# Optimization experiments

Measured on AMD Instinct MI355X. Metric: run time of the kernel, lower is better.

## Reference

```python
import jax, jax.numpy as jnp
import numpy as np

EMBED_DIM = 1024
NUM_HEADS = 16
HEAD_DIM = EMBED_DIM // NUM_HEADS
SEG_LENS = [1024, 2048, 4096]
DIL_RATIOS = [1, 2, 4]
NEG = -1e8  # lse fill value used by sparse_to_dense


def setup_inputs() -> dict:
    root = jax.random.key(0)
    ks = jax.random.split(root, 12)
    B, L, E = 1, 4096, EMBED_DIM
    s = 0.02
    return {
        "query": jax.random.normal(ks[0], (B, L, E), jnp.float32),
        "key": jax.random.normal(ks[1], (B, L, E), jnp.float32),
        "value": jax.random.normal(ks[2], (B, L, E), jnp.float32),
        "Wq": jax.random.normal(ks[3], (E, E), jnp.float32) * s,
        "bq": jnp.zeros((E,), jnp.float32),
        "Wk": jax.random.normal(ks[4], (E, E), jnp.float32) * s,
        "bk": jnp.zeros((E,), jnp.float32),
        "Wv": jax.random.normal(ks[5], (E, E), jnp.float32) * s,
        "bv": jnp.zeros((E,), jnp.float32),
        "Wo": jax.random.normal(ks[6], (E, E), jnp.float32) * s,
        "bo": jnp.zeros((E,), jnp.float32),
    }


def _branch(q, k, v, sl, dr, L):
    """One (segment_length, dilated_ratio) branch.
    q,k,v: (B, L, H, D). Returns dense out (B, H, L, D) and lse (B, H, L).
    """
    B = q.shape[0]
    H, D = NUM_HEADS, HEAD_DIM
    sl = min(sl, L)
    pad = (-L) % sl
    if pad:
        pw = ((0, 0), (0, pad), (0, 0), (0, 0))
        q, k, v = jnp.pad(q, pw), jnp.pad(k, pw), jnp.pad(v, pw)
    n = (L + pad) // sl  # segments
    qs = q.reshape(B * n, sl, H, D)
    ks = k.reshape(B * n, sl, H, D)
    vs = v.reshape(B * n, sl, H, D)
    # dense_to_sparse: head j (group r = j // (H//dr)) keeps positions i*dr + r
    hg = H // dr
    g = sl // dr
    grp = jnp.arange(H) // hg                      # (H,)
    pos = jnp.arange(g)[:, None] * dr + grp[None]  # (g, H) dense positions
    hidx = jnp.arange(H)[None, :]
    sp = lambda x: x[:, pos, hidx, :]              # (B*n, g, H, D)
    qd, kd, vd = sp(qs), sp(ks), sp(vs)
    # causal attention within each sparse segment (flash_attn semantics)
    scores = jnp.einsum('bqhd,bkhd->bhqk', qd, kd) * (D ** -0.5)
    mask = jnp.tril(jnp.ones((g, g), bool))
    scores = jnp.where(mask, scores, -jnp.inf)
    lse = jax.nn.logsumexp(scores, axis=-1)        # (B*n, H, g)
    o = jnp.einsum('bhqk,bkhd->bqhd', jnp.exp(scores - lse[..., None]), vd)
    # sparse_to_dense: scatter back onto dense positions, NEG elsewhere
    hcol = jnp.arange(H)[:, None]                  # (H,1)
    od = jnp.zeros((B * n, H, sl, D), o.dtype).at[:, hcol, pos.T].set(
        o.transpose(0, 2, 1, 3))
    ld = jnp.zeros((B * n, H, sl), lse.dtype).at[:, hcol, pos.T].set(lse)
    ld = jnp.where(ld == 0.0, NEG, ld)  # matches masked_fill_(lse == 0, -1e8)
    od = od.reshape(B, n, H, sl, D).transpose(0, 2, 1, 3, 4)
    od = od.reshape(B, H, n * sl, D)[:, :, :L]
    ld = ld.reshape(B, n, H, sl).transpose(0, 2, 1, 3).reshape(B, H, n * sl)[:, :, :L]
    return od, ld


def reference(query, key, value, Wq, bq, Wk, bk, Wv, bv, Wo, bo):
    B, L, E = query.shape
    H, D = NUM_HEADS, HEAD_DIM
    q = (query @ Wq.T + bq).reshape(B, L, H, D)
    k = (key @ Wk.T + bk).reshape(B, L, H, D)
    v = (value @ Wv.T + bv).reshape(B, L, H, D)
    outs, lses = [], []
    for sl, dr in zip(SEG_LENS, DIL_RATIOS):
        o, l = _branch(q, k, v, sl, dr, L)
        outs.append(o)
        lses.append(l)
    lse_all = jnp.stack(lses, 0)[..., None]        # (nb, B, H, L, 1)
    m = lse_all.max(0)
    w = jnp.exp(lse_all - m)
    w = w / w.sum(0)                               # softmax merge weights
    w = jax.lax.stop_gradient(w)                   # torch computes under no_grad
    out = sum(o * wi.astype(o.dtype) for o, wi in zip(outs, w))  # (B,H,L,D)
    out = out.transpose(0, 2, 1, 3).reshape(B, L, E)
    return out @ Wo.T + bo
```

## Files before the change

kernel.cpp:

```cpp
#include <hip/hip_runtime.h>
#include <math.h>


#define L_SEQ 4096
#define EDIM  1024
#define NH    16
#define HD    64
#define GLEN  1024

typedef __bf16 bf16;
typedef __bf16 bf16x8 __attribute__((ext_vector_type(8)));
typedef __bf16 bf16x4 __attribute__((ext_vector_type(4)));
typedef short  s16x4  __attribute__((ext_vector_type(4)));
typedef float  f32x4  __attribute__((ext_vector_type(4)));

__device__ __forceinline__ void gload16(const bf16* g, bf16* l) {
  __builtin_amdgcn_global_load_lds(
      (__attribute__((address_space(1))) void*)(const_cast<bf16*>(g)),
      (__attribute__((address_space(3))) void*)(l),
      16, 0, 0);
}

__device__ __forceinline__ f32x4 mfma16x16x16_bf16(bf16x4 a, bf16x4 b, f32x4 c) {
#if defined(__HIP_DEVICE_COMPILE__)
  union { bf16x4 h; s16x4 s; } ua, ub;
  ua.h = a; ub.h = b;
  return __builtin_amdgcn_mfma_f32_16x16x16bf16_1k(ua.s, ub.s, c, 0, 0, 0);
#else
  (void)a; (void)b;
  return c;
#endif
}

__global__ __launch_bounds__(256) void cvt_kernel(
    const float* q, const float* k, const float* v,
    const float* wq, const float* wk, const float* wv, const float* wo,
    bf16* oq, bf16* ok, bf16* ov,
    bf16* owq, bf16* owk, bf16* owv, bf16* owo)
{
  const float* src; bf16* dst; int n;
  switch (blockIdx.y) {
    case 0: src = q;  dst = oq;  n = L_SEQ*EDIM; break;
    case 1: src = k;  dst = ok;  n = L_SEQ*EDIM; break;
    case 2: src = v;  dst = ov;  n = L_SEQ*EDIM; break;
    case 3: src = wq; dst = owq; n = EDIM*EDIM; break;
    case 4: src = wk; dst = owk; n = EDIM*EDIM; break;
    case 5: src = wv; dst = owv; n = EDIM*EDIM; break;
    default: src = wo; dst = owo; n = EDIM*EDIM; break;
  }
  int i = (blockIdx.x * 256 + threadIdx.x) * 8;
  if (i >= n) return;
  const float4* s4 = (const float4*)(src + i);
  float4 a = s4[0], b = s4[1];
  bf16x8 o = { (bf16)a.x, (bf16)a.y, (bf16)a.z, (bf16)a.w,
               (bf16)b.x, (bf16)b.y, (bf16)b.z, (bf16)b.w };
  *(bf16x8*)(dst + i) = o;
}

template <typename OutT>
__device__ __forceinline__ void gemm_body(const bf16* __restrict__ A,
                                          const bf16* __restrict__ W,
                                          const float* __restrict__ bias,
                                          OutT* __restrict__ C)
{
  constexpr int K = 1024;
  __shared__ __align__(16) bf16 lA[128 * 32];
  __shared__ __align__(16) bf16 lB[128 * 32];

  const int tid  = threadIdx.x;
  const int lane = tid & 63;
  const int w    = tid >> 6;
  const int quad = lane >> 4;
  const int l16  = lane & 15;
  const int wr   = w >> 1, wc = w & 1;
  const int row0 = blockIdx.y * 128;
  const int col0 = blockIdx.x * 128;

  f32x4 acc[4][4] = {};

  const int c0 = tid, c1 = tid + 256;
  const bf16* Ab0 = A + (size_t)(row0 + (c0 >> 2)) * K + (c0 & 3) * 8;
  const bf16* Ab1 = A + (size_t)(row0 + (c1 >> 2)) * K + (c1 & 3) * 8;
  const bf16* Bb0 = W + (size_t)(col0 + (c0 >> 2)) * K + (c0 & 3) * 8;
  const bf16* Bb1 = W + (size_t)(col0 + (c1 >> 2)) * K + (c1 & 3) * 8;
  bf16* lA0 = &lA[c0 * 8]; bf16* lA1 = &lA[c1 * 8];
  bf16* lB0 = &lB[c0 * 8]; bf16* lB1 = &lB[c1 * 8];

  for (int kt = 0; kt < K; kt += 32) {
    __syncthreads();
    gload16(Ab0 + kt, lA0);
    gload16(Ab1 + kt, lA1);
    gload16(Bb0 + kt, lB0);
    gload16(Bb1 + kt, lB1);
    __syncthreads();

    bf16x8 af[4], bfrag[4];
#pragma unroll
    for (int mi = 0; mi < 4; mi++)
      af[mi] = *(const bf16x8*)&lA[(wr * 64 + mi * 16 + l16) * 32 + quad * 8];
#pragma unroll
    for (int ni = 0; ni < 4; ni++)
      bfrag[ni] = *(const bf16x8*)&lB[(wc * 64 + ni * 16 + l16) * 32 + quad * 8];
#pragma unroll
    for (int mi = 0; mi < 4; mi++)
#pragma unroll
      for (int ni = 0; ni < 4; ni++)
        acc[mi][ni] = __builtin_amdgcn_mfma_f32_16x16x32_bf16(
            af[mi], bfrag[ni], acc[mi][ni], 0, 0, 0);
  }

#pragma unroll
  for (int mi = 0; mi < 4; mi++) {
#pragma unroll
    for (int ni = 0; ni < 4; ni++) {
      const int gcol = col0 + wc * 64 + ni * 16 + l16;
      const float bv = bias[gcol];
#pragma unroll
      for (int r = 0; r < 4; r++) {
        const int grow = row0 + wr * 64 + mi * 16 + quad * 4 + r;
        C[(size_t)grow * 1024 + gcol] = (OutT)(acc[mi][ni][r] + bv);
      }
    }
  }
}

__global__ __launch_bounds__(256) void gemm_qkv_kernel(
    const bf16* xq, const bf16* xk, const bf16* xv,
    const bf16* wq, const bf16* wk, const bf16* wv,
    const float* bq, const float* bk, const float* bv,
    bf16* q, bf16* k, bf16* v)
{
  const bf16 *A, *W; const float* bias; bf16* C;
  if (blockIdx.z == 0)      { A = xq; W = wq; bias = bq; C = q; }
  else if (blockIdx.z == 1) { A = xk; W = wk; bias = bk; C = k; }
  else                      { A = xv; W = wv; bias = bv; C = v; }
  gemm_body<bf16>(A, W, bias, C);
}

__global__ __launch_bounds__(256) void gemm_out_kernel(
    const bf16* A, const bf16* W, const float* bias, float* C)
{
  gemm_body<float>(A, W, bias, C);
}

__global__ __launch_bounds__(256) void reshape_kernel(
    const bf16* __restrict__ k, const bf16* __restrict__ v,
    bf16* kt0, bf16* kt1, bf16* kt2,
    bf16* vt0, bf16* vt1, bf16* vt2)
{
  __shared__ __align__(16) bf16 ltile[64 * 72];
  const int bid = blockIdx.x;
  int sl, dr, rem, shift; bf16 *ktb, *vtb;
  if (bid < 1024)      { sl = 1024; dr = 1; rem = bid;        ktb = kt0; vtb = vt0; shift = 4; }
  else if (bid < 1536) { sl = 2048; dr = 2; rem = bid - 1024; ktb = kt1; vtb = vt1; shift = 3; }
  else                 { sl = 4096; dr = 4; rem = bid - 1536; ktb = kt2; vtb = vt2; shift = 2; }
  const int ktile = rem & 15;
  const int h     = (rem >> 4) & 15;
  const int seg   = rem >> 8;
  const int grp   = h >> shift;
  const int segbase = seg * sl;
  const int tid = threadIdx.x;
  const size_t tOff = ((size_t)((seg * NH + h) * 16 + ktile)) * 4096;

  {
#pragma unroll
    for (int half = 0; half < 2; half++) {
      const int p   = tid + half * 256;
      const int kjl = p >> 3, dc = p & 7;
      const bf16* src = k + (size_t)(segbase + (ktile * 64 + kjl) * dr + grp) * EDIM + h * 64 + dc * 8;
      *(uint4*)(ktb + tOff + p * 8) = *(const uint4*)src;
    }
  }
  {
    const int i = tid >> 2, dc = tid & 3;
    const size_t p = (size_t)(segbase + (ktile * 64 + i) * dr + grp);
    const bf16* src = v + p * EDIM + h * 64 + dc * 16;
    *(uint4*)&ltile[i * 72 + dc * 16]     = *(const uint4*)(src);
    *(uint4*)&ltile[i * 72 + dc * 16 + 8] = *(const uint4*)(src + 8);
  }
  __syncthreads();
  {
    const int d = tid >> 2, kc = tid & 3;
    __align__(16) bf16 tmp[16];
#pragma unroll
    for (int j = 0; j < 16; j++) tmp[j] = ltile[(kc * 16 + j) * 72 + d];
    bf16* dst = vtb + tOff + d * 64 + kc * 16;
    *(uint4*)dst       = *(uint4*)&tmp[0];
    *(uint4*)(dst + 8) = *(uint4*)&tmp[8];
  }
}

__global__ __launch_bounds__(256) void attn_kernel(
    const bf16* __restrict__ qg,
    const bf16* kt0, const bf16* kt1, const bf16* kt2,
    const bf16* vt0, const bf16* vt1, const bf16* vt2,
    bf16* o0, bf16* o1, bf16* o2,
    float* l0, float* l1, float* l2)
{
  __shared__ __align__(16) bf16 lK[64 * 64];
  __shared__ __align__(16) bf16 lV[64 * 64];

  const int bid = blockIdx.x;
  int sl, dr, rem, shift;
  const bf16 *ktb, *vtb; bf16* ob; float* lseb;
  if (bid < 1024)      { sl = 1024; dr = 1; rem = bid;        ktb = kt0; vtb = vt0; ob = o0; lseb = l0; shift = 4; }
  else if (bid < 1536) { sl = 2048; dr = 2; rem = bid - 1024; ktb = kt1; vtb = vt1; ob = o1; lseb = l1; shift = 3; }
  else                 { sl = 4096; dr = 4; rem = bid - 1536; ktb = kt2; vtb = vt2; ob = o2; lseb = l2; shift = 2; }
  const int qt  = 15 - (rem & 15);
  const int h   = (rem >> 4) & 15;
  const int seg = rem >> 8;
  const int grp = h >> shift;
  const int segbase = seg * sl;

  const int tid = threadIdx.x, lane = tid & 63, w = tid >> 6;
  const int quad = lane >> 4, l16 = lane & 15;
  const int qs0 = qt * 64;
  const int qi_lane = qs0 + w * 16 + l16;

  bf16x8 qa0, qa1;
  {
    const size_t p = (size_t)(segbase + qi_lane * dr + grp);
    const bf16* qp = qg + p * EDIM + h * 64 + quad * 8;
    qa0 = *(const bf16x8*)(qp);
    qa1 = *(const bf16x8*)(qp + 32);
  }

  f32x4 Oa[4] = {};
  float m_r = -__builtin_inff(), l_r = 0.f;

  const bf16* kbase = ktb + ((size_t)((seg * NH + h) * 16)) * 4096;
  const bf16* vbase = vtb + ((size_t)((seg * NH + h) * 16)) * 4096;

  const int p0 = tid, p1 = tid + 256;
  const int s0 = (p0 >> 3) * 64 + (((p0 & 7) ^ ((p0 >> 3) & 7)) * 8);
  const int s1 = (p1 >> 3) * 64 + (((p1 & 7) ^ ((p1 >> 3) & 7)) * 8);

  uint4 rk0 = *(const uint4*)(kbase + p0 * 8);
  uint4 rk1 = *(const uint4*)(kbase + p1 * 8);
  uint4 rv0 = *(const uint4*)(vbase + p0 * 8);
  uint4 rv1 = *(const uint4*)(vbase + p1 * 8);

  for (int kt = 0; kt <= qt; kt++) {
    __syncthreads();
    *(uint4*)&lK[s0] = rk0;
    *(uint4*)&lK[s1] = rk1;
    *(uint4*)&lV[s0] = rv0;
    *(uint4*)&lV[s1] = rv1;
    if (kt < qt) {
      const bf16* kT = kbase + (size_t)(kt + 1) * 4096;
      const bf16* vT = vbase + (size_t)(kt + 1) * 4096;
      rk0 = *(const uint4*)(kT + p0 * 8);
      rk1 = *(const uint4*)(kT + p1 * 8);
      rv0 = *(const uint4*)(vT + p0 * 8);
      rv1 = *(const uint4*)(vT + p1 * 8);
    }
    __syncthreads();

    const bool diag = (kt == qt);
    const int tmax = diag ? w : 3;

    f32x4 s[4];
#pragma unroll
    for (int t = 0; t < 4; t++) {
      if (t <= tmax) {
        s[t] = f32x4{0.f, 0.f, 0.f, 0.f};
        const int kj = t * 16 + l16;
        const int rs = kj & 7;
        bf16x8 ka0 = *(const bf16x8*)&lK[kj * 64 + ((quad       ^ rs) * 8)];
        bf16x8 ka1 = *(const bf16x8*)&lK[kj * 64 + (((4 + quad) ^ rs) * 8)];
        s[t] = __builtin_amdgcn_mfma_f32_16x16x32_bf16(ka0, qa0, s[t], 0, 0, 0);
        s[t] = __builtin_amdgcn_mfma_f32_16x16x32_bf16(ka1, qa1, s[t], 0, 0, 0);
      }
    }

    float p[4][4];
    float mloc = -__builtin_inff();
#pragma unroll
    for (int t = 0; t < 4; t++) {
      if (t <= tmax) {
#pragma unroll
        for (int r = 0; r < 4; r++) {
          float sv = s[t][r] * 0.125f;
          if (diag) {
            const int kj = kt * 64 + t * 16 + quad * 4 + r;
            if (kj > qi_lane) sv = -__builtin_inff();
          }
          p[t][r] = sv;
          mloc = fmaxf(mloc, sv);
        }
      }
    }
    mloc = fmaxf(mloc, __shfl_xor(mloc, 16, 64));
    mloc = fmaxf(mloc, __shfl_xor(mloc, 32, 64));
    const float mnew  = fmaxf(m_r, mloc);
    const float alpha = __expf(m_r - mnew);
    m_r = mnew;

    bf16x4 pb[4];
    float rs_sum = 0.f;
#pragma unroll
    for (int t = 0; t < 4; t++) {
      if (t <= tmax) {
#pragma unroll
        for (int r = 0; r < 4; r++) {
          const float pv = __expf(p[t][r] - mnew);
          pb[t][r] = (bf16)pv;
          rs_sum += pv;
        }
      }
    }
    rs_sum += __shfl_xor(rs_sum, 16, 64);
    rs_sum += __shfl_xor(rs_sum, 32, 64);
    l_r = l_r * alpha + rs_sum;

#pragma unroll
    for (int nf = 0; nf < 4; nf++) {
#pragma unroll
      for (int r = 0; r < 4; r++) Oa[nf][r] *= alpha;
    }

#pragma unroll
    for (int t = 0; t < 4; t++) {
      if (t <= tmax) {
        const int ck  = 2 * t + (quad >> 1);
        const int sub = (quad & 1) * 4;
#pragma unroll
        for (int nf = 0; nf < 4; nf++) {
          const int drow = nf * 16 + l16;
          bf16x4 va = *(const bf16x4*)&lV[drow * 64 + ((ck ^ (drow & 7)) * 8) + sub];
          Oa[nf] = mfma16x16x16_bf16(va, pb[t], Oa[nf]);
        }
      }
    }
  }

  const float linv = 1.0f / l_r;
  const int pdense = segbase + qi_lane * dr + grp;
  bf16* orow = ob + (size_t)pdense * EDIM + h * 64;
#pragma unroll
  for (int nf = 0; nf < 4; nf++) {
    bf16x4 ov;
#pragma unroll
    for (int r = 0; r < 4; r++) ov[r] = (bf16)(Oa[nf][r] * linv);
    *(bf16x4*)(orow + nf * 16 + quad * 4) = ov;
  }
  if (quad == 0)
    lseb[h * L_SEQ + pdense] = m_r + __logf(l_r);
}

__global__ __launch_bounds__(256) void merge_kernel(
    const bf16* __restrict__ o0, const bf16* __restrict__ o1, const bf16* __restrict__ o2,
    const float* __restrict__ l0, const float* __restrict__ l1, const float* __restrict__ l2,
    bf16* __restrict__ merged)
{
  const int idx = blockIdx.x * 256 + threadIdx.x;
  const int dc = idx & 7;
  const int h  = (idx >> 3) & 15;
  const int p  = idx >> 7;
  const bool c1 = ((p & 1) == (h >> 3));
  const bool c2 = ((p & 3) == (h >> 2));
  const float s0 = l0[h * L_SEQ + p];
  const float s1 = c1 ? l1[h * L_SEQ + p] : -__builtin_inff();
  const float s2 = c2 ? l2[h * L_SEQ + p] : -__builtin_inff();
  const float mx = fmaxf(s0, fmaxf(s1, s2));
  float w0 = __expf(s0 - mx);
  float w1 = c1 ? __expf(s1 - mx) : 0.f;
  float w2 = c2 ? __expf(s2 - mx) : 0.f;
  const float inv = 1.0f / (w0 + w1 + w2);
  w0 *= inv; w1 *= inv; w2 *= inv;

  const size_t off = (size_t)p * EDIM + h * 64 + dc * 8;
  float acc[8];
  bf16x8 a0 = *(const bf16x8*)(o0 + off);
#pragma unroll
  for (int j = 0; j < 8; j++) acc[j] = w0 * (float)a0[j];
  if (c1) {
    bf16x8 a1 = *(const bf16x8*)(o1 + off);
#pragma unroll
    for (int j = 0; j < 8; j++) acc[j] += w1 * (float)a1[j];
  }
  if (c2) {
    bf16x8 a2 = *(const bf16x8*)(o2 + off);
#pragma unroll
    for (int j = 0; j < 8; j++) acc[j] += w2 * (float)a2[j];
  }
  bf16x8 r;
#pragma unroll
  for (int j = 0; j < 8; j++) r[j] = (bf16)acc[j];
  *(bf16x8*)(merged + off) = r;
}

extern "C" void kernel_launch(void* const* d_in, const int* in_sizes, int n_in,
                              void* d_out, int out_size, void* d_ws, size_t ws_size,
                              hipStream_t stream)
{
  (void)in_sizes; (void)n_in; (void)out_size; (void)ws_size;
  const float* query = (const float*)d_in[0];
  const float* key   = (const float*)d_in[1];
  const float* value = (const float*)d_in[2];
  const float* Wq = (const float*)d_in[3];
  const float* bq = (const float*)d_in[4];
  const float* Wk = (const float*)d_in[5];
  const float* bk = (const float*)d_in[6];
  const float* Wv = (const float*)d_in[7];
  const float* bv = (const float*)d_in[8];
  const float* Wo = (const float*)d_in[9];
  const float* bo = (const float*)d_in[10];

  char* base = (char*)d_ws;
  size_t off = 0;
  auto take = [&](size_t nbytes) -> char* {
    char* p = base + off;
    off += (nbytes + 255) & ~(size_t)255;
    return p;
  };
  const size_t LE2 = (size_t)L_SEQ * EDIM * 2;
  const size_t EE2 = (size_t)EDIM * EDIM * 2;
  bf16* xq  = (bf16*)take(LE2);
  bf16* xk  = (bf16*)take(LE2);
  bf16* xv  = (bf16*)take(LE2);
  bf16* wqb = (bf16*)take(EE2);
  bf16* wkb = (bf16*)take(EE2);
  bf16* wvb = (bf16*)take(EE2);
  bf16* wob = (bf16*)take(EE2);
  bf16* qb  = (bf16*)take(LE2);
  bf16* kb  = (bf16*)take(LE2);
  bf16* vb  = (bf16*)take(LE2);
  bf16* kt0 = (bf16*)take((size_t)4 * NH * GLEN * HD * 2);
  bf16* kt1 = (bf16*)take((size_t)2 * NH * GLEN * HD * 2);
  bf16* kt2 = (bf16*)take((size_t)1 * NH * GLEN * HD * 2);
  bf16* vt0 = (bf16*)take((size_t)4 * NH * HD * GLEN * 2);
  bf16* vt1 = (bf16*)take((size_t)2 * NH * HD * GLEN * 2);
  bf16* vt2 = (bf16*)take((size_t)1 * NH * HD * GLEN * 2);
  float* lse0 = (float*)take((size_t)NH * L_SEQ * 4);
  float* lse1 = (float*)take((size_t)NH * L_SEQ * 4);
  float* lse2 = (float*)take((size_t)NH * L_SEQ * 4);
  bf16* merged = (bf16*)take(LE2);
  bf16* o0 = xq; bf16* o1 = xk; bf16* o2 = xv;

  dim3 blk(256);
  cvt_kernel<<<dim3(2048, 7), blk, 0, stream>>>(
      query, key, value, Wq, Wk, Wv, Wo, xq, xk, xv, wqb, wkb, wvb, wob);
  gemm_qkv_kernel<<<dim3(8, 32, 3), blk, 0, stream>>>(
      xq, xk, xv, wqb, wkb, wvb, bq, bk, bv, qb, kb, vb);
  reshape_kernel<<<dim3(1792), blk, 0, stream>>>(
      kb, vb, kt0, kt1, kt2, vt0, vt1, vt2);
  attn_kernel<<<dim3(1792), blk, 0, stream>>>(
      qb, kt0, kt1, kt2, vt0, vt1, vt2, o0, o1, o2, lse0, lse1, lse2);
  merge_kernel<<<dim3(2048), blk, 0, stream>>>(
      o0, o1, o2, lse0, lse1, lse2, merged);
  gemm_out_kernel<<<dim3(8, 32), blk, 0, stream>>>(merged, wob, bo, (float*)d_out);
}
```

Before: 262.0 us.

## Process two query tiles per attention block and double-buffer K/V in LDS

```diff
diff --git a/kernel.cpp b/kernel.cpp
--- a/kernel.cpp
+++ b/kernel.cpp
@@ -197,36 +197,42 @@
     bf16* o0, bf16* o1, bf16* o2,
     float* l0, float* l1, float* l2)
 {
-  __shared__ __align__(16) bf16 lK[64 * 64];
-  __shared__ __align__(16) bf16 lV[64 * 64];
+  __shared__ __align__(16) bf16 lK[2][64 * 64];
+  __shared__ __align__(16) bf16 lV[2][64 * 64];
 
   const int bid = blockIdx.x;
   int sl, dr, rem, shift;
   const bf16 *ktb, *vtb; bf16* ob; float* lseb;
-  if (bid < 1024)      { sl = 1024; dr = 1; rem = bid;        ktb = kt0; vtb = vt0; ob = o0; lseb = l0; shift = 4; }
-  else if (bid < 1536) { sl = 2048; dr = 2; rem = bid - 1024; ktb = kt1; vtb = vt1; ob = o1; lseb = l1; shift = 3; }
-  else                 { sl = 4096; dr = 4; rem = bid - 1536; ktb = kt2; vtb = vt2; ob = o2; lseb = l2; shift = 2; }
-  const int qt  = 15 - (rem & 15);
-  const int h   = (rem >> 4) & 15;
-  const int seg = rem >> 8;
+  if (bid < 512)       { sl = 1024; dr = 1; rem = bid;       ktb = kt0; vtb = vt0; ob = o0; lseb = l0; shift = 4; }
+  else if (bid < 768)  { sl = 2048; dr = 2; rem = bid - 512; ktb = kt1; vtb = vt1; ob = o1; lseb = l1; shift = 3; }
+  else                 { sl = 4096; dr = 4; rem = bid - 768; ktb = kt2; vtb = vt2; ob = o2; lseb = l2; shift = 2; }
+  const int qt2 = 7 - (rem & 7);
+  const int h   = (rem >> 3) & 15;
+  const int seg = rem >> 7;
   const int grp = h >> shift;
   const int segbase = seg * sl;
 
   const int tid = threadIdx.x, lane = tid & 63, w = tid >> 6;
   const int quad = lane >> 4, l16 = lane & 15;
-  const int qs0 = qt * 64;
-  const int qi_lane = qs0 + w * 16 + l16;
-
-  bf16x8 qa0, qa1;
-  {
-    const size_t p = (size_t)(segbase + qi_lane * dr + grp);
+  const int ktd0 = 2 * qt2;
+  const int ktmx = 2 * qt2 + 1;
+
+  int qi[2];
+  qi[0] = qt2 * 128 + w * 16 + l16;
+  qi[1] = qi[0] + 64;
+
+  bf16x8 qa[2][2];
+#pragma unroll
+  for (int g = 0; g < 2; g++) {
+    const size_t p = (size_t)(segbase + qi[g] * dr + grp);
     const bf16* qp = qg + p * EDIM + h * 64 + quad * 8;
-    qa0 = *(const bf16x8*)(qp);
-    qa1 = *(const bf16x8*)(qp + 32);
-  }
-
-  f32x4 Oa[4] = {};
-  float m_r = -__builtin_inff(), l_r = 0.f;
+    qa[g][0] = *(const bf16x8*)(qp);
+    qa[g][1] = *(const bf16x8*)(qp + 32);
+  }
+
+  f32x4 Oa[2][4] = {};
+  float m_r[2] = { -__builtin_inff(), -__builtin_inff() };
+  float l_r[2] = { 0.f, 0.f };
 
   const bf16* kbase = ktb + ((size_t)((seg * NH + h) * 16)) * 4096;
   const bf16* vbase = vtb + ((size_t)((seg * NH + h) * 16)) * 4096;
@@ -239,113 +245,152 @@
   uint4 rk1 = *(const uint4*)(kbase + p1 * 8);
   uint4 rv0 = *(const uint4*)(vbase + p0 * 8);
   uint4 rv1 = *(const uint4*)(vbase + p1 * 8);
-
-  for (int kt = 0; kt <= qt; kt++) {
+  *(uint4*)&lK[0][s0] = rk0;
+  *(uint4*)&lK[0][s1] = rk1;
+  *(uint4*)&lV[0][s0] = rv0;
+  *(uint4*)&lV[0][s1] = rv1;
+  {
+    const bf16* kT = kbase + 4096;
+    const bf16* vT = vbase + 4096;
+    rk0 = *(const uint4*)(kT + p0 * 8);
+    rk1 = *(const uint4*)(kT + p1 * 8);
+    rv0 = *(const uint4*)(vT + p0 * 8);
+    rv1 = *(const uint4*)(vT + p1 * 8);
+  }
+
+  for (int kt = 0; kt <= ktmx; kt++) {
     __syncthreads();
-    *(uint4*)&lK[s0] = rk0;
-    *(uint4*)&lK[s1] = rk1;
-    *(uint4*)&lV[s0] = rv0;
-    *(uint4*)&lV[s1] = rv1;
-    if (kt < qt) {
-      const bf16* kT = kbase + (size_t)(kt + 1) * 4096;
-      const bf16* vT = vbase + (size_t)(kt + 1) * 4096;
-      rk0 = *(const uint4*)(kT + p0 * 8);
-      rk1 = *(const uint4*)(kT + p1 * 8);
-      rv0 = *(const uint4*)(vT + p0 * 8);
-      rv1 = *(const uint4*)(vT + p1 * 8);
-    }
-    __syncthreads();
-
-    const bool diag = (kt == qt);
-    const int tmax = diag ? w : 3;
-
-    f32x4 s[4];
+    const bf16* bK = lK[kt & 1];
+    const bf16* bV = lV[kt & 1];
+
+    const bool last = (kt == ktmx);
+    const int tK = last ? w : 3;
+
+    f32x4 s[2][4];
+    const bool act0 = (kt <= ktd0);
+    const int tmax0 = (kt == ktd0) ? w : 3;
+    const int tmax1 = last ? w : 3;
 #pragma unroll
     for (int t = 0; t < 4; t++) {
-      if (t <= tmax) {
-        s[t] = f32x4{0.f, 0.f, 0.f, 0.f};
+      if (t <= tK) {
         const int kj = t * 16 + l16;
         const int rs = kj & 7;
-        bf16x8 ka0 = *(const bf16x8*)&lK[kj * 64 + ((quad       ^ rs) * 8)];
-        bf16x8 ka1 = *(const bf16x8*)&lK[kj * 64 + (((4 + quad) ^ rs) * 8)];
-        s[t] = __builtin_amdgcn_mfma_f32_16x16x32_bf16(ka0, qa0, s[t], 0, 0, 0);
-        s[t] = __builtin_amdgcn_mfma_f32_16x16x32_bf16(ka1, qa1, s[t], 0, 0, 0);
-      }
-    }
-
-    float p[4][4];
-    float mloc = -__builtin_inff();
+        bf16x8 ka0 = *(const bf16x8*)&bK[kj * 64 + ((quad       ^ rs) * 8)];
+        bf16x8 ka1 = *(const bf16x8*)&bK[kj * 64 + (((4 + quad) ^ rs) * 8)];
+        if (act0 && t <= tmax0) {
+          f32x4 z = {0.f, 0.f, 0.f, 0.f};
+          z = __builtin_amdgcn_mfma_f32_16x16x32_bf16(ka0, qa[0][0], z, 0, 0, 0);
+          s[0][t] = __builtin_amdgcn_mfma_f32_16x16x32_bf16(ka1, qa[0][1], z, 0, 0, 0);
+        }
+        {
+          f32x4 z = {0.f, 0.f, 0.f, 0.f};
+          z = __builtin_amdgcn_mfma_f32_16x16x32_bf16(ka0, qa[1][0], z, 0, 0, 0);
+          s[1][t] = __builtin_amdgcn_mfma_f32_16x16x32_bf16(ka1, qa[1][1], z, 0, 0, 0);
+        }
+      }
+    }
+
+    bf16x4 pb[2][4];
+#pragma unroll
+    for (int g = 0; g < 2; g++) {
+      const bool act  = (g == 0) ? act0 : true;
+      if (!act) continue;
+      const bool diag = (kt == (g ? ktmx : ktd0));
+      const int tmax  = (g == 0) ? tmax0 : tmax1;
+      float p[4][4];
+      float mloc = -__builtin_inff();
+#pragma unroll
+      for (int t = 0; t < 4; t++) {
+        if (t <= tmax) {
+#pragma unroll
+          for (int r = 0; r < 4; r++) {
+            float sv = s[g][t][r] * 0.125f;
+            if (diag) {
+              const int kj = kt * 64 + t * 16 + quad * 4 + r;
+              if (kj > qi[g]) sv = -__builtin_inff();
+            }
+            p[t][r] = sv;
+            mloc = fmaxf(mloc, sv);
+          }
+        }
+      }
+      mloc = fmaxf(mloc, __shfl_xor(mloc, 16, 64));
+      mloc = fmaxf(mloc, __shfl_xor(mloc, 32, 64));
+      const float mnew  = fmaxf(m_r[g], mloc);
+      const float alpha = __expf(m_r[g] - mnew);
+      m_r[g] = mnew;
+
+      float rs_sum = 0.f;
+#pragma unroll
+      for (int t = 0; t < 4; t++) {
+        if (t <= tmax) {
+#pragma unroll
+          for (int r = 0; r < 4; r++) {
+            const float pv = __expf(p[t][r] - mnew);
+            pb[g][t][r] = (bf16)pv;
+            rs_sum += pv;
+          }
+        }
+      }
+      rs_sum += __shfl_xor(rs_sum, 16, 64);
+      rs_sum += __shfl_xor(rs_sum, 32, 64);
+      l_r[g] = l_r[g] * alpha + rs_sum;
+
+#pragma unroll
+      for (int nf = 0; nf < 4; nf++)
+#pragma unroll
+        for (int r = 0; r < 4; r++) Oa[g][nf][r] *= alpha;
+    }
+
 #pragma unroll
     for (int t = 0; t < 4; t++) {
-      if (t <= tmax) {
-#pragma unroll
-        for (int r = 0; r < 4; r++) {
-          float sv = s[t][r] * 0.125f;
-          if (diag) {
-            const int kj = kt * 64 + t * 16 + quad * 4 + r;
-            if (kj > qi_lane) sv = -__builtin_inff();
-          }
-          p[t][r] = sv;
-          mloc = fmaxf(mloc, sv);
-        }
-      }
-    }
-    mloc = fmaxf(mloc, __shfl_xor(mloc, 16, 64));
-    mloc = fmaxf(mloc, __shfl_xor(mloc, 32, 64));
-    const float mnew  = fmaxf(m_r, mloc);
-    const float alpha = __expf(m_r - mnew);
-    m_r = mnew;
-
-    bf16x4 pb[4];
-    float rs_sum = 0.f;
-#pragma unroll
-    for (int t = 0; t < 4; t++) {
-      if (t <= tmax) {
-#pragma unroll
-        for (int r = 0; r < 4; r++) {
-          const float pv = __expf(p[t][r] - mnew);
-          pb[t][r] = (bf16)pv;
-          rs_sum += pv;
-        }
-      }
-    }
-    rs_sum += __shfl_xor(rs_sum, 16, 64);
-    rs_sum += __shfl_xor(rs_sum, 32, 64);
-    l_r = l_r * alpha + rs_sum;
-
-#pragma unroll
-    for (int nf = 0; nf < 4; nf++) {
-#pragma unroll
-      for (int r = 0; r < 4; r++) Oa[nf][r] *= alpha;
-    }
-
-#pragma unroll
-    for (int t = 0; t < 4; t++) {
-      if (t <= tmax) {
+      if (t <= tK) {
         const int ck  = 2 * t + (quad >> 1);
         const int sub = (quad & 1) * 4;
 #pragma unroll
         for (int nf = 0; nf < 4; nf++) {
           const int drow = nf * 16 + l16;
-          bf16x4 va = *(const bf16x4*)&lV[drow * 64 + ((ck ^ (drow & 7)) * 8) + sub];
-          Oa[nf] = mfma16x16x16_bf16(va, pb[t], Oa[nf]);
+          bf16x4 va = *(const bf16x4*)&bV[drow * 64 + ((ck ^ (drow & 7)) * 8) + sub];
+          if (act0 && t <= tmax0)
+            Oa[0][nf] = mfma16x16x16_bf16(va, pb[0][t], Oa[0][nf]);
+          if (t <= tmax1)
+            Oa[1][nf] = mfma16x16x16_bf16(va, pb[1][t], Oa[1][nf]);
         }
       }
     }
-  }
-
-  const float linv = 1.0f / l_r;
-  const int pdense = segbase + qi_lane * dr + grp;
-  bf16* orow = ob + (size_t)pdense * EDIM + h * 64;
-#pragma unroll
-  for (int nf = 0; nf < 4; nf++) {
-    bf16x4 ov;
-#pragma unroll
-    for (int r = 0; r < 4; r++) ov[r] = (bf16)(Oa[nf][r] * linv);
-    *(bf16x4*)(orow + nf * 16 + quad * 4) = ov;
-  }
-  if (quad == 0)
-    lseb[h * L_SEQ + pdense] = m_r + __logf(l_r);
+
+    if (kt < ktmx) {
+      const int nb = (kt + 1) & 1;
+      *(uint4*)&lK[nb][s0] = rk0;
+      *(uint4*)&lK[nb][s1] = rk1;
+      *(uint4*)&lV[nb][s0] = rv0;
+      *(uint4*)&lV[nb][s1] = rv1;
+      if (kt + 1 < ktmx) {
+        const bf16* kT = kbase + (size_t)(kt + 2) * 4096;
+        const bf16* vT = vbase + (size_t)(kt + 2) * 4096;
+        rk0 = *(const uint4*)(kT + p0 * 8);
+        rk1 = *(const uint4*)(kT + p1 * 8);
+        rv0 = *(const uint4*)(vT + p0 * 8);
+        rv1 = *(const uint4*)(vT + p1 * 8);
+      }
+    }
+  }
+
+#pragma unroll
+  for (int g = 0; g < 2; g++) {
+    const float linv = 1.0f / l_r[g];
+    const int pdense = segbase + qi[g] * dr + grp;
+    bf16* orow = ob + (size_t)pdense * EDIM + h * 64;
+#pragma unroll
+    for (int nf = 0; nf < 4; nf++) {
+      bf16x4 ov;
+#pragma unroll
+      for (int r = 0; r < 4; r++) ov[r] = (bf16)(Oa[g][nf][r] * linv);
+      *(bf16x4*)(orow + nf * 16 + quad * 4) = ov;
+    }
+    if (quad == 0)
+      lseb[h * L_SEQ + pdense] = m_r[g] + __logf(l_r[g]);
+  }
 }
 
 __global__ __launch_bounds__(256) void merge_kernel(
@@ -445,7 +490,7 @@
       xq, xk, xv, wqb, wkb, wvb, bq, bk, bv, qb, kb, vb);
   reshape_kernel<<<dim3(1792), blk, 0, stream>>>(
       kb, vb, kt0, kt1, kt2, vt0, vt1, vt2);
-  attn_kernel<<<dim3(1792), blk, 0, stream>>>(
+  attn_kernel<<<dim3(896), blk, 0, stream>>>(
       qb, kt0, kt1, kt2, vt0, vt1, vt2, o0, o1, o2, lse0, lse1, lse2);
   merge_kernel<<<dim3(2048), blk, 0, stream>>>(
       o0, o1, o2, lse0, lse1, lse2, merged);
```

New measurement: 272.0 us. +3.8%, slower.

## Split attention into single-wave blocks loading K/V directly to registers

Applied to the files above, without the earlier changes.

```diff
diff --git a/kernel.cpp b/kernel.cpp
--- a/kernel.cpp
+++ b/kernel.cpp
@@ -190,86 +190,84 @@
   }
 }
 
-__global__ __launch_bounds__(256) void attn_kernel(
+__global__ __launch_bounds__(64, 3) void attn_kernel(
     const bf16* __restrict__ qg,
     const bf16* kt0, const bf16* kt1, const bf16* kt2,
     const bf16* vt0, const bf16* vt1, const bf16* vt2,
     bf16* o0, bf16* o1, bf16* o2,
     float* l0, float* l1, float* l2)
 {
-  __shared__ __align__(16) bf16 lK[64 * 64];
-  __shared__ __align__(16) bf16 lV[64 * 64];
-
   const int bid = blockIdx.x;
-  int sl, dr, rem, shift;
+  const int xcd = bid & 7;
+  const int pos = bid >> 3;
+  const int item = pos / 14;
+  const int gi   = pos % 14;
+  const int g    = gi * 8 + xcd;
+
+  int seg, h, sl, dr, shift;
   const bf16 *ktb, *vtb; bf16* ob; float* lseb;
-  if (bid < 1024)      { sl = 1024; dr = 1; rem = bid;        ktb = kt0; vtb = vt0; ob = o0; lseb = l0; shift = 4; }
-  else if (bid < 1536) { sl = 2048; dr = 2; rem = bid - 1024; ktb = kt1; vtb = vt1; ob = o1; lseb = l1; shift = 3; }
-  else                 { sl = 4096; dr = 4; rem = bid - 1536; ktb = kt2; vtb = vt2; ob = o2; lseb = l2; shift = 2; }
-  const int qt  = 15 - (rem & 15);
-  const int h   = (rem >> 4) & 15;
-  const int seg = rem >> 8;
+  if (g < 64)      { seg = g >> 4;        h = g & 15;        sl = 1024; dr = 1; shift = 4; ktb = kt0; vtb = vt0; ob = o0; lseb = l0; }
+  else if (g < 96) { seg = (g - 64) >> 4; h = (g - 64) & 15; sl = 2048; dr = 2; shift = 3; ktb = kt1; vtb = vt1; ob = o1; lseb = l1; }
+  else             { seg = 0;             h = (g - 96) & 15; sl = 4096; dr = 4; shift = 2; ktb = kt2; vtb = vt2; ob = o2; lseb = l2; }
   const int grp = h >> shift;
   const int segbase = seg * sl;
 
-  const int tid = threadIdx.x, lane = tid & 63, w = tid >> 6;
+  const int qtt = 15 - (item >> 2);
+  const int sub = item & 3;
+  const int qrs = qtt * 64 + sub * 16;
+  const int ktd = qtt;
+
+  const int lane = threadIdx.x;
   const int quad = lane >> 4, l16 = lane & 15;
-  const int qs0 = qt * 64;
-  const int qi_lane = qs0 + w * 16 + l16;
+  const int qi = qrs + l16;
 
   bf16x8 qa0, qa1;
   {
-    const size_t p = (size_t)(segbase + qi_lane * dr + grp);
+    const size_t p = (size_t)(segbase + qi * dr + grp);
     const bf16* qp = qg + p * EDIM + h * 64 + quad * 8;
     qa0 = *(const bf16x8*)(qp);
     qa1 = *(const bf16x8*)(qp + 32);
   }
 
+  const bf16* kbase = ktb + ((size_t)((seg * NH + h) * 16)) * 4096;
+  const bf16* vbase = vtb + ((size_t)((seg * NH + h) * 16)) * 4096;
+  const int koff = l16 * 64 + quad * 8;
+  const int voff = l16 * 64 + quad * 4;
+
   f32x4 Oa[4] = {};
   float m_r = -__builtin_inff(), l_r = 0.f;
 
-  const bf16* kbase = ktb + ((size_t)((seg * NH + h) * 16)) * 4096;
-  const bf16* vbase = vtb + ((size_t)((seg * NH + h) * 16)) * 4096;
-
-  const int p0 = tid, p1 = tid + 256;
-  const int s0 = (p0 >> 3) * 64 + (((p0 & 7) ^ ((p0 >> 3) & 7)) * 8);
-  const int s1 = (p1 >> 3) * 64 + (((p1 & 7) ^ ((p1 >> 3) & 7)) * 8);
-
-  uint4 rk0 = *(const uint4*)(kbase + p0 * 8);
-  uint4 rk1 = *(const uint4*)(kbase + p1 * 8);
-  uint4 rv0 = *(const uint4*)(vbase + p0 * 8);
-  uint4 rv1 = *(const uint4*)(vbase + p1 * 8);
-
-  for (int kt = 0; kt <= qt; kt++) {
-    __syncthreads();
-    *(uint4*)&lK[s0] = rk0;
-    *(uint4*)&lK[s1] = rk1;
-    *(uint4*)&lV[s0] = rv0;
-    *(uint4*)&lV[s1] = rv1;
-    if (kt < qt) {
-      const bf16* kT = kbase + (size_t)(kt + 1) * 4096;
-      const bf16* vT = vbase + (size_t)(kt + 1) * 4096;
-      rk0 = *(const uint4*)(kT + p0 * 8);
-      rk1 = *(const uint4*)(kT + p1 * 8);
-      rv0 = *(const uint4*)(vT + p0 * 8);
-      rv1 = *(const uint4*)(vT + p1 * 8);
-    }
-    __syncthreads();
-
-    const bool diag = (kt == qt);
-    const int tmax = diag ? w : 3;
+  bf16x8 kA[8], kB[8];
+  bf16x4 vv[16];
+
+  auto loadK = [&](int kt, bf16x8* kr) {
+    const bf16* kT = kbase + (size_t)kt * 4096 + koff;
+#pragma unroll
+    for (int t = 0; t < 4; t++) {
+      kr[2 * t]     = *(const bf16x8*)(kT + t * 1024);
+      kr[2 * t + 1] = *(const bf16x8*)(kT + t * 1024 + 32);
+    }
+  };
+  auto loadV = [&](int kt) {
+    const bf16* vT = vbase + (size_t)kt * 4096 + voff;
+#pragma unroll
+    for (int nf = 0; nf < 4; nf++)
+#pragma unroll
+      for (int t = 0; t < 4; t++)
+        vv[nf * 4 + t] = *(const bf16x4*)(vT + nf * 1024 + t * 16);
+  };
+
+  auto compute = [&](int kt, const bf16x8* kr) {
+    const bool diag = (kt == ktd);
+    const int tmax = diag ? sub : 3;
 
     f32x4 s[4];
 #pragma unroll
     for (int t = 0; t < 4; t++) {
       if (t <= tmax) {
-        s[t] = f32x4{0.f, 0.f, 0.f, 0.f};
-        const int kj = t * 16 + l16;
-        const int rs = kj & 7;
-        bf16x8 ka0 = *(const bf16x8*)&lK[kj * 64 + ((quad       ^ rs) * 8)];
-        bf16x8 ka1 = *(const bf16x8*)&lK[kj * 64 + (((4 + quad) ^ rs) * 8)];
-        s[t] = __builtin_amdgcn_mfma_f32_16x16x32_bf16(ka0, qa0, s[t], 0, 0, 0);
-        s[t] = __builtin_amdgcn_mfma_f32_16x16x32_bf16(ka1, qa1, s[t], 0, 0, 0);
+        f32x4 z = {0.f, 0.f, 0.f, 0.f};
+        z    = __builtin_amdgcn_mfma_f32_16x16x32_bf16(kr[2 * t],     qa0, z, 0, 0, 0);
+        s[t] = __builtin_amdgcn_mfma_f32_16x16x32_bf16(kr[2 * t + 1], qa1, z, 0, 0, 0);
       }
     }
 
@@ -281,9 +279,8 @@
 #pragma unroll
         for (int r = 0; r < 4; r++) {
           float sv = s[t][r] * 0.125f;
-          if (diag) {
-            const int kj = kt * 64 + t * 16 + quad * 4 + r;
-            if (kj > qi_lane) sv = -__builtin_inff();
+          if (diag && t == tmax) {
+            if (quad * 4 + r > l16) sv = -__builtin_inff();
           }
           p[t][r] = sv;
           mloc = fmaxf(mloc, sv);
@@ -314,28 +311,35 @@
     l_r = l_r * alpha + rs_sum;
 
 #pragma unroll
-    for (int nf = 0; nf < 4; nf++) {
+    for (int nf = 0; nf < 4; nf++)
 #pragma unroll
       for (int r = 0; r < 4; r++) Oa[nf][r] *= alpha;
-    }
 
 #pragma unroll
     for (int t = 0; t < 4; t++) {
       if (t <= tmax) {
-        const int ck  = 2 * t + (quad >> 1);
-        const int sub = (quad & 1) * 4;
-#pragma unroll
-        for (int nf = 0; nf < 4; nf++) {
-          const int drow = nf * 16 + l16;
-          bf16x4 va = *(const bf16x4*)&lV[drow * 64 + ((ck ^ (drow & 7)) * 8) + sub];
-          Oa[nf] = mfma16x16x16_bf16(va, pb[t], Oa[nf]);
-        }
+#pragma unroll
+        for (int nf = 0; nf < 4; nf++)
+          Oa[nf] = mfma16x16x16_bf16(vv[nf * 4 + t], pb[t], Oa[nf]);
       }
     }
+  };
+
+  loadK(0, kA);
+#pragma unroll 1
+  for (int kt = 0; kt <= ktd; kt += 2) {
+    loadV(kt);
+    if (kt < ktd) loadK(kt + 1, kB);
+    compute(kt, kA);
+    if (kt + 1 <= ktd) {
+      loadV(kt + 1);
+      if (kt + 2 <= ktd) loadK(kt + 2, kA);
+      compute(kt + 1, kB);
+    }
   }
 
   const float linv = 1.0f / l_r;
-  const int pdense = segbase + qi_lane * dr + grp;
+  const int pdense = segbase + qi * dr + grp;
   bf16* orow = ob + (size_t)pdense * EDIM + h * 64;
 #pragma unroll
   for (int nf = 0; nf < 4; nf++) {
@@ -445,7 +449,7 @@
       xq, xk, xv, wqb, wkb, wvb, bq, bk, bv, qb, kb, vb);
   reshape_kernel<<<dim3(1792), blk, 0, stream>>>(
       kb, vb, kt0, kt1, kt2, vt0, vt1, vt2);
-  attn_kernel<<<dim3(1792), blk, 0, stream>>>(
+  attn_kernel<<<dim3(7168), dim3(64), 0, stream>>>(
       qb, kt0, kt1, kt2, vt0, vt1, vt2, o0, o1, o2, lse0, lse1, lse2);
   merge_kernel<<<dim3(2048), blk, 0, stream>>>(
       o0, o1, o2, lse0, lse1, lse2, merged);
```

Result: slower. 357.3 us (+36.4%).
